# Performance work log

Hardware: AMD Instinct MI355X
Metric: run time of the kernel (lower is better)

The kernel has to match this reference:

```python
import jax, jax.numpy as jnp
import numpy as np
import itertools

N = 65536          # points
R = 1.0 / 16.0     # radius (forward uses 1/16)
K = 64             # max_num_neighbors in forward call
G = 16             # grid cells per axis (cell size == R)


def _radius_knn_edges(pts):
    """Grid-hashed radius search; per point keep nearest K within R (self-loop included),
    pad with self index so every point has exactly K edges (max-aggregation neutral)."""
    cells = np.minimum((pts / R).astype(np.int64), G - 1)
    cid = (cells[:, 0] * G + cells[:, 1]) * G + cells[:, 2]
    order = np.argsort(cid, kind='stable')
    sorted_cid = cid[order]
    counts = np.bincount(cid, minlength=G ** 3)
    starts = np.concatenate([[0], np.cumsum(counts)[:-1]])
    M = int(counts.max())
    cand = -np.ones((G ** 3, M), dtype=np.int64)
    slot = np.arange(N) - starts[sorted_cid]
    cand[sorted_cid, slot] = order
    offs = np.array(list(itertools.product([-1, 0, 1], repeat=3)))
    nbr = np.empty((N, K), dtype=np.int64)
    chunk = 4096
    for s in range(0, N, chunk):
        e = min(s + chunk, N)
        c = cells[s:e]
        nc = c[:, None, :] + offs[None]                      # [B,27,3]
        valid_c = np.all((nc >= 0) & (nc < G), axis=-1)      # [B,27]
        ncid = (nc[..., 0] * G + nc[..., 1]) * G + nc[..., 2]
        ncid = np.where(valid_c, ncid, 0)
        cd = cand[ncid]                                      # [B,27,M]
        cd = np.where(np.broadcast_to(valid_c[..., None], cd.shape), cd, -1)
        cd = cd.reshape(e - s, -1)                           # [B,27M]
        p = pts[np.maximum(cd, 0)]
        d = np.linalg.norm(p - pts[s:e, None, :], axis=-1)
        d = np.where((cd >= 0) & (d <= R), d, np.inf)
        sel = np.argsort(d, axis=1)[:, :K]
        row = np.arange(e - s)[:, None]
        picked = cd[row, sel]
        ok = np.isfinite(d[row, sel])
        nbr[s:e] = np.where(ok, picked, np.arange(s, e)[:, None])
    out_index = np.repeat(np.arange(N, dtype=np.int64), K)
    in_index = nbr.reshape(-1)
    return out_index, in_index


def setup_inputs() -> dict:
    key = jax.random.key(0)
    ks = jax.random.split(key, 16)
    pos = jax.random.uniform(ks[0], (N, 3), dtype=jnp.float32)
    rgb = jax.random.uniform(ks[1], (N, 3), dtype=jnp.float32)
    batch = jnp.zeros((N,), dtype=jnp.int64)
    oi, ii = _radius_knn_edges(np.asarray(pos, dtype=np.float64))
    out_index = jnp.asarray(oi)
    in_index = jnp.asarray(ii)

    def lin_w(k, fi, fo):
        return jax.random.normal(k, (fi, fo), dtype=jnp.float32) / np.sqrt(fi).astype(np.float32)

    def lin_b(k, fo):
        return 0.01 * jax.random.normal(k, (fo,), dtype=jnp.float32)

    return {
        'pos': pos, 'rgb': rgb, 'batch': batch,
        'out_index': out_index, 'in_index': in_index,
        'w1a': lin_w(ks[2], 6, 8),   'b1a': lin_b(ks[3], 8),
        'w1b': lin_w(ks[4], 8, 8),   'b1b': lin_b(ks[5], 8),
        'w2a': lin_w(ks[6], 11, 16), 'b2a': lin_b(ks[7], 16),
        'w2b': lin_w(ks[8], 16, 16), 'b2b': lin_b(ks[9], 16),
        'w3a': lin_w(ks[10], 19, 32), 'b3a': lin_b(ks[11], 32),
        'w3b': lin_w(ks[12], 32, 32), 'b3b': lin_b(ks[13], 32),
    }


def _point_conv(x, pos, out_index, in_index, wa, ba, wb, bb):
    # gather neighbor features + relative position, local MLP, max-scatter, output linear
    dpos = pos[in_index] - pos[out_index]                      # [E,3]
    msg = jnp.concatenate([x[in_index], dpos], axis=-1)        # [E,c_in+3]
    h = jax.nn.celu(msg @ wa + ba)                             # [E,c_mid]
    agg = jax.ops.segment_max(h, out_index, num_segments=pos.shape[0],
                              indices_are_sorted=True)         # [N,c_mid]
    return agg @ wb + bb                                       # [N,c_out]


def reference(pos, rgb, batch, out_index, in_index,
              w1a, b1a, w1b, b1b, w2a, b2a, w2b, b2b, w3a, b3a, w3b, b3b):
    out = jax.nn.celu(_point_conv(pos, pos, out_index, in_index, w1a, b1a, w1b, b1b))
    out = jax.nn.celu(_point_conv(out, pos, out_index, in_index, w2a, b2a, w2b, b2b))
    out = jax.nn.celu(_point_conv(out, pos, out_index, in_index, w3a, b3a, w3b, b3b))
    return (pos, out, batch)
```

## Files before the change

kernel.cpp:

```cpp
#include <hip/hip_runtime.h>
#include <hip/hip_fp16.h>
#include <math.h>


#define NPTS 65536
#define KNBR 64

__device__ __forceinline__ float celu1(float x) {
    return x > 0.0f ? x : (__expf(x) - 1.0f);
}

__device__ __forceinline__ void max2(float& a, float& b, unsigned u) {
    __half2 h = *(__half2*)&u;
    float2 f = __half22float2(h);
    a = fmaxf(a, f.x);
    b = fmaxf(b, f.y);
}

__device__ __forceinline__ unsigned pack2(float a, float b) {
    __half2 h = __floats2half2_rn(a, b);
    return *(unsigned*)&h;
}

__global__ __launch_bounds__(256) void k_prep1(
    const float* __restrict__ pos,
    const float* __restrict__ w1a,
    const float* __restrict__ b1a,
    __half* __restrict__ q1,
    float* __restrict__ dout,
    int out_size)
{
    int t = blockIdx.x * 256 + threadIdx.x;
    if (t >= NPTS) return;
    float p0 = pos[3 * t + 0];
    float p1 = pos[3 * t + 1];
    float p2 = pos[3 * t + 2];
    dout[3 * t + 0] = p0;
    dout[3 * t + 1] = p1;
    dout[3 * t + 2] = p2;
    float q[8];
#pragma unroll
    for (int c = 0; c < 8; ++c) {
        float a = b1a[c];
        a = fmaf(p0, w1a[0 * 8 + c] + w1a[3 * 8 + c], a);
        a = fmaf(p1, w1a[1 * 8 + c] + w1a[4 * 8 + c], a);
        a = fmaf(p2, w1a[2 * 8 + c] + w1a[5 * 8 + c], a);
        q[c] = a;
    }
    uint4 pk;
    pk.x = pack2(q[0], q[1]);
    pk.y = pack2(q[2], q[3]);
    pk.z = pack2(q[4], q[5]);
    pk.w = pack2(q[6], q[7]);
    *(uint4*)(q1 + 8 * t) = pk;
    for (int j = 35 * NPTS + t; j < out_size; j += NPTS)
        dout[j] = 0.0f;
}

template <int FH>
__global__ __launch_bounds__(256) void k_edge(
    const __half* __restrict__ q,
    const int* __restrict__ idx,
    float* __restrict__ m)
{
    int gt = blockIdx.x * 256 + threadIdx.x;
    int p = gt >> 3;
    int s = gt & 7;
    float mx[FH];
#pragma unroll
    for (int c = 0; c < FH; ++c) mx[c] = -3.0e38f;

    int base = p * KNBR + s;
#pragma unroll 2
    for (int e = 0; e < KNBR / 8; ++e) {
        int j = idx[base + e * 8];
        const uint4* qr = (const uint4*)(q + j * FH);
#pragma unroll
        for (int l = 0; l < FH / 8; ++l) {
            uint4 v = qr[l];
            max2(mx[l * 8 + 0], mx[l * 8 + 1], v.x);
            max2(mx[l * 8 + 2], mx[l * 8 + 3], v.y);
            max2(mx[l * 8 + 4], mx[l * 8 + 5], v.z);
            max2(mx[l * 8 + 6], mx[l * 8 + 7], v.w);
        }
    }
#pragma unroll
    for (int st = 1; st < 8; st <<= 1) {
#pragma unroll
        for (int c = 0; c < FH; ++c)
            mx[c] = fmaxf(mx[c], __shfl_xor(mx[c], st, 64));
    }
    constexpr int CW = FH / 8;
    float outv[CW];
#pragma unroll
    for (int c = 0; c < CW; ++c) {
        float v = mx[c];
#pragma unroll
        for (int g = 1; g < 8; ++g)
            v = (s == g) ? mx[g * CW + c] : v;
        outv[c] = v;
    }
    float* dst = m + p * FH + s * CW;
    if constexpr (CW == 4) {
        *(float4*)dst = make_float4(outv[0], outv[1], outv[2], outv[3]);
    } else if constexpr (CW == 2) {
        *(float2*)dst = make_float2(outv[0], outv[1]);
    } else {
        *dst = outv[0];
    }
}

template <int FH, int FOUT, int FHN, bool WRITEX>
__global__ __launch_bounds__(256) void k_finish(
    const float* __restrict__ m,
    const float* __restrict__ pos,
    const float* __restrict__ wap,
    const float* __restrict__ wb,
    const float* __restrict__ bb,
    const float* __restrict__ wan,
    const float* __restrict__ ban,
    float* __restrict__ xout,
    __half* __restrict__ qnext)
{
    int t = blockIdx.x * 256 + threadIdx.x;
    float p0 = pos[3 * t + 0];
    float p1 = pos[3 * t + 1];
    float p2 = pos[3 * t + 2];

    float h[FH];
    const float4* mr = (const float4*)(m + t * FH);
#pragma unroll
    for (int c4 = 0; c4 < FH / 4; ++c4) {
        float4 v = mr[c4];
        h[4 * c4 + 0] = v.x;
        h[4 * c4 + 1] = v.y;
        h[4 * c4 + 2] = v.z;
        h[4 * c4 + 3] = v.w;
    }
#pragma unroll
    for (int c = 0; c < FH; ++c) {
        float g = p0 * wap[c] + p1 * wap[FH + c] + p2 * wap[2 * FH + c];
        h[c] = celu1(h[c] - g);
    }
    float x[FOUT];
#pragma unroll
    for (int c2 = 0; c2 < FOUT; ++c2) {
        float a = bb[c2];
#pragma unroll
        for (int c = 0; c < FH; ++c)
            a = fmaf(h[c], wb[c * FOUT + c2], a);
        x[c2] = celu1(a);
    }
    if constexpr (WRITEX) {
        float4* xo = (float4*)(xout + t * FOUT);
#pragma unroll
        for (int c4 = 0; c4 < FOUT / 4; ++c4)
            xo[c4] = make_float4(x[4 * c4 + 0], x[4 * c4 + 1], x[4 * c4 + 2], x[4 * c4 + 3]);
    }
    if constexpr (FHN > 0) {
        float qn[FHN];
#pragma unroll
        for (int cn = 0; cn < FHN; ++cn) {
            float a = ban[cn];
#pragma unroll
            for (int c2 = 0; c2 < FOUT; ++c2)
                a = fmaf(x[c2], wan[c2 * FHN + cn], a);
            a = fmaf(p0, wan[(FOUT + 0) * FHN + cn], a);
            a = fmaf(p1, wan[(FOUT + 1) * FHN + cn], a);
            a = fmaf(p2, wan[(FOUT + 2) * FHN + cn], a);
            qn[cn] = a;
        }
        uint4* qo = (uint4*)(qnext + t * FHN);
#pragma unroll
        for (int l = 0; l < FHN / 8; ++l) {
            uint4 pk;
            pk.x = pack2(qn[l * 8 + 0], qn[l * 8 + 1]);
            pk.y = pack2(qn[l * 8 + 2], qn[l * 8 + 3]);
            pk.z = pack2(qn[l * 8 + 4], qn[l * 8 + 5]);
            pk.w = pack2(qn[l * 8 + 6], qn[l * 8 + 7]);
            qo[l] = pk;
        }
    }
}

extern "C" void kernel_launch(void* const* d_in, const int* in_sizes, int n_in,
                              void* d_out, int out_size, void* d_ws, size_t ws_size,
                              hipStream_t stream) {
    const float* pos = (const float*)d_in[0];
    const int* idx = (const int*)d_in[4];
    const float* w1a = (const float*)d_in[5];
    const float* b1a = (const float*)d_in[6];
    const float* w1b = (const float*)d_in[7];
    const float* b1b = (const float*)d_in[8];
    const float* w2a = (const float*)d_in[9];
    const float* b2a = (const float*)d_in[10];
    const float* w2b = (const float*)d_in[11];
    const float* b2b = (const float*)d_in[12];
    const float* w3a = (const float*)d_in[13];
    const float* b3a = (const float*)d_in[14];
    const float* w3b = (const float*)d_in[15];
    const float* b3b = (const float*)d_in[16];
    float* out = (float*)d_out;

    char* ws = (char*)d_ws;
    __half* A = (__half*)ws;
    float*  B = (float*)(ws + 8u * 1024u * 1024u);

    k_prep1<<<NPTS / 256, 256, 0, stream>>>(pos, w1a, b1a, A, out, out_size);
    k_edge<8><<<NPTS * 8 / 256, 256, 0, stream>>>(A, idx, B);
    k_finish<8, 8, 16, false><<<NPTS / 256, 256, 0, stream>>>(
        B, pos, w1a + 3 * 8, w1b, b1b, w2a, b2a, nullptr, A);
    k_edge<16><<<NPTS * 8 / 256, 256, 0, stream>>>(A, idx, B);
    k_finish<16, 16, 32, false><<<NPTS / 256, 256, 0, stream>>>(
        B, pos, w2a + 8 * 16, w2b, b2b, w3a, b3a, nullptr, A);
    k_edge<32><<<NPTS * 8 / 256, 256, 0, stream>>>(A, idx, B);
    k_finish<32, 32, 0, true><<<NPTS / 256, 256, 0, stream>>>(
        B, pos, w3a + 16 * 32, w3b, b3b, nullptr, nullptr, out + 3 * NPTS, nullptr);
}
```

Baseline: 210.9 us.

## Restructure edge max-gather with packed fp16 max, vector index loads, fp16 output

The edge kernel is remapped so each wave handles 4 points with 16 lanes each. Each lane loads its neighbor indices as uint4 vectors and reads a 16-byte feature slice per neighbor. The max is kept in packed fp16 via v_pk_max_f16 instead of converting to float. The lane reduction uses fewer shuffles, and the aggregated result is written as fp16, halving the intermediate buffer traffic that k_finish reads back. The aim is to cut index-load instructions, conversion ALU work and memory traffic. It ties the code to inline AMD assembly, and fp16 rounding of the aggregate was already present in the inputs.

```diff
diff --git a/kernel.cpp b/kernel.cpp
--- a/kernel.cpp
+++ b/kernel.cpp
@@ -10,11 +10,10 @@
     return x > 0.0f ? x : (__expf(x) - 1.0f);
 }
 
-__device__ __forceinline__ void max2(float& a, float& b, unsigned u) {
-    __half2 h = *(__half2*)&u;
-    float2 f = __half22float2(h);
-    a = fmaxf(a, f.x);
-    b = fmaxf(b, f.y);
+__device__ __forceinline__ unsigned pkmax(unsigned a, unsigned b) {
+    unsigned d;
+    asm("v_pk_max_f16 %0, %1, %2" : "=v"(d) : "v"(a), "v"(b));
+    return d;
 }
 
 __device__ __forceinline__ unsigned pack2(float a, float b) {
@@ -61,58 +60,54 @@
 __global__ __launch_bounds__(256) void k_edge(
     const __half* __restrict__ q,
     const int* __restrict__ idx,
-    float* __restrict__ m)
+    __half* __restrict__ m)
 {
-    int gt = blockIdx.x * 256 + threadIdx.x;
-    int p = gt >> 3;
-    int s = gt & 7;
-    float mx[FH];
-#pragma unroll
-    for (int c = 0; c < FH; ++c) mx[c] = -3.0e38f;
-
-    int base = p * KNBR + s;
-#pragma unroll 2
-    for (int e = 0; e < KNBR / 8; ++e) {
-        int j = idx[base + e * 8];
-        const uint4* qr = (const uint4*)(q + j * FH);
-#pragma unroll
-        for (int l = 0; l < FH / 8; ++l) {
-            uint4 v = qr[l];
-            max2(mx[l * 8 + 0], mx[l * 8 + 1], v.x);
-            max2(mx[l * 8 + 2], mx[l * 8 + 3], v.y);
-            max2(mx[l * 8 + 4], mx[l * 8 + 5], v.z);
-            max2(mx[l * 8 + 6], mx[l * 8 + 7], v.w);
-        }
-    }
-#pragma unroll
-    for (int st = 1; st < 8; st <<= 1) {
-#pragma unroll
-        for (int c = 0; c < FH; ++c)
-            mx[c] = fmaxf(mx[c], __shfl_xor(mx[c], st, 64));
-    }
-    constexpr int CW = FH / 8;
-    float outv[CW];
-#pragma unroll
-    for (int c = 0; c < CW; ++c) {
-        float v = mx[c];
-#pragma unroll
-        for (int g = 1; g < 8; ++g)
-            v = (s == g) ? mx[g * CW + c] : v;
-        outv[c] = v;
-    }
-    float* dst = m + p * FH + s * CW;
-    if constexpr (CW == 4) {
-        *(float4*)dst = make_float4(outv[0], outv[1], outv[2], outv[3]);
-    } else if constexpr (CW == 2) {
-        *(float2*)dst = make_float2(outv[0], outv[1]);
-    } else {
-        *dst = outv[0];
+    constexpr int SL  = FH / 8;
+    constexpr int EG  = 16 / SL;
+    constexpr int EPG = 64 / EG;
+
+    int wave = (blockIdx.x * 256 + threadIdx.x) >> 6;
+    int l  = threadIdx.x & 63;
+    int pl = l >> 4;
+    int u  = l & 15;
+    int c  = u % SL;
+    int g  = u / SL;
+    int p  = wave * 4 + pl;
+
+    const uint4* ip = (const uint4*)(idx + p * KNBR + g * EPG);
+    uint4 iv[EPG / 4];
+#pragma unroll
+    for (int k = 0; k < EPG / 4; ++k) iv[k] = ip[k];
+
+    unsigned ax = 0xFC00FC00u, ay = 0xFC00FC00u, az = 0xFC00FC00u, aw = 0xFC00FC00u;
+#pragma unroll
+    for (int k = 0; k < EPG / 4; ++k) {
+        int j0 = (int)iv[k].x, j1 = (int)iv[k].y, j2 = (int)iv[k].z, j3 = (int)iv[k].w;
+        uint4 v0 = *(const uint4*)(q + j0 * FH + c * 8);
+        uint4 v1 = *(const uint4*)(q + j1 * FH + c * 8);
+        uint4 v2 = *(const uint4*)(q + j2 * FH + c * 8);
+        uint4 v3 = *(const uint4*)(q + j3 * FH + c * 8);
+        ax = pkmax(ax, v0.x); ay = pkmax(ay, v0.y); az = pkmax(az, v0.z); aw = pkmax(aw, v0.w);
+        ax = pkmax(ax, v1.x); ay = pkmax(ay, v1.y); az = pkmax(az, v1.z); aw = pkmax(aw, v1.w);
+        ax = pkmax(ax, v2.x); ay = pkmax(ay, v2.y); az = pkmax(az, v2.z); aw = pkmax(aw, v2.w);
+        ax = pkmax(ax, v3.x); ay = pkmax(ay, v3.y); az = pkmax(az, v3.z); aw = pkmax(aw, v3.w);
+    }
+#pragma unroll
+    for (int st = SL; st < 16; st <<= 1) {
+        ax = pkmax(ax, (unsigned)__shfl_xor((int)ax, st, 64));
+        ay = pkmax(ay, (unsigned)__shfl_xor((int)ay, st, 64));
+        az = pkmax(az, (unsigned)__shfl_xor((int)az, st, 64));
+        aw = pkmax(aw, (unsigned)__shfl_xor((int)aw, st, 64));
+    }
+    if (g == 0) {
+        uint4 r; r.x = ax; r.y = ay; r.z = az; r.w = aw;
+        *(uint4*)(m + p * FH + c * 8) = r;
     }
 }
 
 template <int FH, int FOUT, int FHN, bool WRITEX>
 __global__ __launch_bounds__(256) void k_finish(
-    const float* __restrict__ m,
+    const __half* __restrict__ m,
     const float* __restrict__ pos,
     const float* __restrict__ wap,
     const float* __restrict__ wb,
@@ -128,14 +123,17 @@
     float p2 = pos[3 * t + 2];
 
     float h[FH];
-    const float4* mr = (const float4*)(m + t * FH);
-#pragma unroll
-    for (int c4 = 0; c4 < FH / 4; ++c4) {
-        float4 v = mr[c4];
-        h[4 * c4 + 0] = v.x;
-        h[4 * c4 + 1] = v.y;
-        h[4 * c4 + 2] = v.z;
-        h[4 * c4 + 3] = v.w;
+    const uint4* mr = (const uint4*)(m + t * FH);
+#pragma unroll
+    for (int l = 0; l < FH / 8; ++l) {
+        uint4 v = mr[l];
+        unsigned w4[4] = {v.x, v.y, v.z, v.w};
+#pragma unroll
+        for (int k = 0; k < 4; ++k) {
+            float2 f = __half22float2(*(__half2*)&w4[k]);
+            h[l * 8 + k * 2 + 0] = f.x;
+            h[l * 8 + k * 2 + 1] = f.y;
+        }
     }
 #pragma unroll
     for (int c = 0; c < FH; ++c) {
@@ -204,16 +202,16 @@
 
     char* ws = (char*)d_ws;
     __half* A = (__half*)ws;
-    float*  B = (float*)(ws + 8u * 1024u * 1024u);
+    __half* B = (__half*)(ws + 8u * 1024u * 1024u);
 
     k_prep1<<<NPTS / 256, 256, 0, stream>>>(pos, w1a, b1a, A, out, out_size);
-    k_edge<8><<<NPTS * 8 / 256, 256, 0, stream>>>(A, idx, B);
+    k_edge<8><<<NPTS / 16, 256, 0, stream>>>(A, idx, B);
     k_finish<8, 8, 16, false><<<NPTS / 256, 256, 0, stream>>>(
         B, pos, w1a + 3 * 8, w1b, b1b, w2a, b2a, nullptr, A);
-    k_edge<16><<<NPTS * 8 / 256, 256, 0, stream>>>(A, idx, B);
+    k_edge<16><<<NPTS / 16, 256, 0, stream>>>(A, idx, B);
     k_finish<16, 16, 32, false><<<NPTS / 256, 256, 0, stream>>>(
         B, pos, w2a + 8 * 16, w2b, b2b, w3a, b3a, nullptr, A);
-    k_edge<32><<<NPTS * 8 / 256, 256, 0, stream>>>(A, idx, B);
+    k_edge<32><<<NPTS / 16, 256, 0, stream>>>(A, idx, B);
     k_finish<32, 32, 0, true><<<NPTS / 256, 256, 0, stream>>>(
         B, pos, w3a + 16 * 32, w3b, b3b, nullptr, nullptr, out + 3 * NPTS, nullptr);
 }
```

Result: faster. 193.9 us (-8.1%).
